# Kernel optimization log

Hardware: AMD Instinct MI355X
Metric: run time of the kernel (lower is better)

## Reference

```python
import jax, jax.numpy as jnp
import numpy as np

B, C, W = 8, 128, 4096
REDUCTION = 8
D = C // REDUCTION  # 16


def setup_inputs() -> dict:
    key = jax.random.key(0)
    ks = jax.random.split(key, 7)
    scale = 0.05
    return {
        "x": jax.random.normal(ks[0], (B, C, W), dtype=jnp.float32),
        "Wq": jax.random.normal(ks[1], (D, C), dtype=jnp.float32) * scale,
        "bq": jax.random.normal(ks[2], (D,), dtype=jnp.float32) * scale,
        "Wk": jax.random.normal(ks[3], (D, C), dtype=jnp.float32) * scale,
        "bk": jax.random.normal(ks[4], (D,), dtype=jnp.float32) * scale,
        "Wv": jax.random.normal(ks[5], (C, C), dtype=jnp.float32) * scale,
        "bv": jax.random.normal(ks[6], (C,), dtype=jnp.float32) * scale,
    }


def reference(x, Wq, bq, Wk, bk, Wv, bv):
    # 1x1 Conv1d == per-position linear over channel axis
    q = jnp.einsum('dc,bcw->bdw', Wq, x) + bq[None, :, None]   # [B, D, W]
    k = jnp.einsum('dc,bcw->bdw', Wk, x) + bk[None, :, None]   # [B, D, W]
    v = jnp.einsum('oc,bcw->bow', Wv, x) + bv[None, :, None]   # [B, C, W]
    scale = D ** (-0.5)
    # scores[b,i,j] = q[b,:,i] . k[b,:,j]
    scores = jnp.einsum('bdi,bdj->bij', q, k) * scale          # [B, W, W]
    attn = jax.nn.softmax(scores, axis=-1)
    # torch.bmm(value, attn): context[b,c,w] = sum_j v[b,c,j] * attn[b,j,w]
    context = jnp.einsum('bcj,bjw->bcw', v, attn)              # [B, C, W]
    return context + x
```

## Files before the change

kernel.cpp:

```cpp
#include <hip/hip_runtime.h>

#define B_ 8
#define C_ 128
#define W_ 4096
#define D_ 16
#define SCALE2 0.3606737602222409f

typedef short bf16x8 __attribute__((ext_vector_type(8)));
typedef float f32x4 __attribute__((ext_vector_type(4)));
typedef float f32x16 __attribute__((ext_vector_type(16)));

__device__ __forceinline__ unsigned short f2bf(float f) {
    unsigned int u = __float_as_uint(f);
    u += 0x7fffu + ((u >> 16) & 1u);
    return (unsigned short)(u >> 16);
}
__device__ __forceinline__ float bf2f(unsigned short h) {
    return __uint_as_float(((unsigned int)h) << 16);
}
__device__ __forceinline__ unsigned int pk2bf(float lo, float hi) {
    return __builtin_amdgcn_perm(__float_as_uint(hi), __float_as_uint(lo), 0x07060302u);
}
__device__ __forceinline__ bf16x8 uint4_as_bf8(uint4 u) {
    union { uint4 u; bf16x8 v; } t;
    t.u = u;
    return t.v;
}
__device__ __forceinline__ bf16x8 ld8w(const float* p, float sc) {
    float4 lo = *(const float4*)p, hi = *(const float4*)(p + 4);
    union { uint4 u; bf16x8 v; } t;
    t.u = make_uint4(pk2bf(lo.x * sc, lo.y * sc), pk2bf(lo.z * sc, lo.w * sc),
                     pk2bf(hi.x * sc, hi.y * sc), pk2bf(hi.z * sc, hi.w * sc));
    return t.v;
}
__device__ __forceinline__ uint4 exp2pkq(f32x16 s, int r0) {
    return make_uint4(
        pk2bf(__builtin_amdgcn_exp2f(s[r0+0]), __builtin_amdgcn_exp2f(s[r0+1])),
        pk2bf(__builtin_amdgcn_exp2f(s[r0+2]), __builtin_amdgcn_exp2f(s[r0+3])),
        pk2bf(__builtin_amdgcn_exp2f(s[r0+4]), __builtin_amdgcn_exp2f(s[r0+5])),
        pk2bf(__builtin_amdgcn_exp2f(s[r0+6]), __builtin_amdgcn_exp2f(s[r0+7])));
}
__device__ __forceinline__ int xswz(int j, int c8) {
    return c8 ^ (j & 7) ^ ((j >> 3) & 7);
}

__global__ __launch_bounds__(256) void proj(
    const float* __restrict__ x,
    const float* __restrict__ Wq, const float* __restrict__ Wk, const float* __restrict__ Wv,
    const float* __restrict__ bqp, const float* __restrict__ bkp, const float* __restrict__ bvp,
    unsigned short* __restrict__ qws2, unsigned short* __restrict__ kws2,
    unsigned short* __restrict__ vws2)
{
    __shared__ unsigned short xbf[32 * 128];
    __shared__ unsigned short outs[128 * 36];
    __shared__ unsigned short qk_s[2][32][24];

    int b  = blockIdx.x & 7;
    int j0 = (blockIdx.x >> 3) * 32;
    int jt = j0 >> 5;
    int tid = threadIdx.x;
    int wid = tid >> 6, lane = tid & 63, n = lane & 15, q4 = lane >> 4;

    {
        unsigned int* xbf32 = (unsigned int*)xbf;
#pragma unroll
        for (int i = 0; i < 8; i++) {
            int p = tid + 256 * i;
            int c2 = p >> 5;
            int j  = p & 31;
            const float* xp = x + (size_t)(b * C_ + 2 * c2) * W_ + j0 + j;
            float lo = xp[0];
            float hi = xp[W_];
            xbf32[j * 64 + xswz(j, c2 >> 2) * 4 + (c2 & 3)] = pk2bf(lo, hi);
        }
    }
    __syncthreads();

    const f32x4 zero = {0.f, 0.f, 0.f, 0.f};
    f32x4 accv[2][2]; f32x4 accqk = zero;
#pragma unroll
    for (int os = 0; os < 2; os++)
#pragma unroll
        for (int js = 0; js < 2; js++) accv[os][js] = zero;

    int isK = wid >> 1;
    int jsm = wid & 1;
    const float* wqk = isK ? Wk : Wq;
    const float qksc = isK ? 1.0f : SCALE2;

#pragma unroll
    for (int kk = 0; kk < 128; kk += 32) {
        bf16x8 av[2], aqkf, bx[2];
#pragma unroll
        for (int os = 0; os < 2; os++)
            av[os] = ld8w(Wv + (size_t)(wid * 32 + os * 16 + n) * 128 + kk + q4 * 8, 1.0f);
        aqkf = ld8w(wqk + (size_t)n * 128 + kk + q4 * 8, qksc);
#pragma unroll
        for (int js = 0; js < 2; js++) {
            int j = js * 16 + n;
            bx[js] = *(const bf16x8*)&xbf[j * 128 + xswz(j, (kk >> 3) + q4) * 8];
        }
#pragma unroll
        for (int os = 0; os < 2; os++)
#pragma unroll
            for (int js = 0; js < 2; js++)
                accv[os][js] = __builtin_amdgcn_mfma_f32_16x16x32_bf16(av[os], bx[js], accv[os][js], 0, 0, 0);
        accqk = __builtin_amdgcn_mfma_f32_16x16x32_bf16(aqkf, bx[jsm], accqk, 0, 0, 0);
    }

    {
        int pos = jsm * 16 + n;
        const float* bias = isK ? bkp : bqp;
        float bsc = isK ? 1.0f : SCALE2;
#pragma unroll
        for (int r = 0; r < 4; r++)
            qk_s[isK][pos][q4 * 4 + r] = f2bf(accqk[r] + bias[q4 * 4 + r] * bsc);
    }

    float bvv[2][4];
#pragma unroll
    for (int os = 0; os < 2; os++)
#pragma unroll
        for (int r = 0; r < 4; r++) bvv[os][r] = bvp[wid * 32 + os * 16 + q4 * 4 + r];
#pragma unroll
    for (int os = 0; os < 2; os++)
#pragma unroll
        for (int js = 0; js < 2; js++)
#pragma unroll
            for (int r = 0; r < 4; r++) {
                int c = wid * 32 + os * 16 + q4 * 4 + r;
                int j = js * 16 + n;
                outs[c * 36 + j] = f2bf(accv[os][js][r] + bvv[os][r]);
            }
    __syncthreads();

    if (tid < 128) {
        int qk = tid >> 6, hh = (tid >> 5) & 1, jl = tid & 31;
        uint4 v = *(const uint4*)&qk_s[qk][jl][hh * 8];
        unsigned short* dst = (qk ? kws2 : qws2)
            + (size_t)(b * 128 + jt) * 512 + hh * 256 + jl * 8;
        *(uint4*)dst = v;
    }
#pragma unroll
    for (int rep = 0; rep < 2; rep++) {
        int t = tid + rep * 256;
        int c = t & 127, sel = t >> 7;
        int jb = (sel >> 1) * 16 + (sel & 1) * 4;
        uint2 lo = *(const uint2*)&outs[c * 36 + jb];
        uint2 hi = *(const uint2*)&outs[c * 36 + jb + 8];
        *(uint4*)(vws2 + ((size_t)(b * 128 + jt) * 4 + sel) * 1024 + c * 8) =
            make_uint4(lo.x, lo.y, hi.x, hi.y);
    }
}

__global__ __launch_bounds__(256) void row_stats(
    const unsigned short* __restrict__ qws2, const unsigned short* __restrict__ kws2,
    float* __restrict__ rlp)
{
    int blk = blockIdx.x;
    int b = blk & 7;
    int j0 = ((blk >> 3) & 31) * 128;
    int wsp = blk >> 8;
    int tid = threadIdx.x;
    int wid = tid >> 6, lane = tid & 63, wl = lane & 31, h = lane >> 5;

    const unsigned short* qb = qws2 + (size_t)b * 65536;
    const unsigned short* kb = kws2 + (size_t)b * 65536;
    int jt = (j0 >> 5) + wid;

    bf16x8 aq = *(const bf16x8*)(qb + (size_t)jt * 512 + h * 256 + wl * 8);
    f32x16 zero16 = {0.f,0.f,0.f,0.f,0.f,0.f,0.f,0.f,0.f,0.f,0.f,0.f,0.f,0.f,0.f,0.f};

    float lt[16];
#pragma unroll
    for (int r = 0; r < 16; r++) lt[r] = 0.f;

    bf16x8 bkc = *(const bf16x8*)(kb + (size_t)(wsp * 32) * 512 + h * 256 + wl * 8);
    for (int t = 0; t < 32; t++) {
        f32x16 s = __builtin_amdgcn_mfma_f32_32x32x16_bf16(aq, bkc, zero16, 0, 0, 0);
        int tn = wsp * 32 + ((t + 1) & 31);
        bkc = *(const bf16x8*)(kb + (size_t)tn * 512 + h * 256 + wl * 8);
#pragma unroll
        for (int r = 0; r < 16; r++) lt[r] += __builtin_amdgcn_exp2f(s[r]);
    }
#pragma unroll
    for (int mask = 1; mask < 32; mask <<= 1)
#pragma unroll
        for (int r = 0; r < 16; r++) lt[r] += __shfl_xor(lt[r], mask, 64);
    if (wl == 0) {
#pragma unroll
        for (int g = 0; g < 4; g++) {
            f32x4 v = {lt[4*g+0], lt[4*g+1], lt[4*g+2], lt[4*g+3]};
            *(f32x4*)(rlp + (size_t)wsp * 32768 + (size_t)b * W_ + j0 + wid * 32 + 4 * h + 8 * g) = v;
        }
    }
}

__global__ __launch_bounds__(256) void vscale(unsigned short* __restrict__ vws2,
                                              const float* __restrict__ rlp)
{
    __shared__ float rl[16];
    int bi = blockIdx.x;
    int g0 = bi * 256;
    int kf = (g0 >> 8) & 1, jt = (g0 >> 9) & 127, b = g0 >> 16;
    int tid = threadIdx.x;
    if (tid < 16) {
        int idx = b * W_ + jt * 32 + kf * 16 + tid;
        float l = rlp[idx] + rlp[32768 + idx] + rlp[65536 + idx] + rlp[98304 + idx];
        rl[tid] = 1.0f / l;
    }
    __syncthreads();

    int g = g0 + tid;
    int hh = (g >> 7) & 1;
    float4 r0 = *(const float4*)&rl[4 * hh];
    float4 r1 = *(const float4*)&rl[4 * hh + 8];
    uint4 v = *(const uint4*)(vws2 + (size_t)g * 8);
    unsigned int o0 = pk2bf(bf2f((unsigned short)(v.x & 0xffffu)) * r0.x,
                            bf2f((unsigned short)(v.x >> 16))     * r0.y);
    unsigned int o1 = pk2bf(bf2f((unsigned short)(v.y & 0xffffu)) * r0.z,
                            bf2f((unsigned short)(v.y >> 16))     * r0.w);
    unsigned int o2 = pk2bf(bf2f((unsigned short)(v.z & 0xffffu)) * r1.x,
                            bf2f((unsigned short)(v.z >> 16))     * r1.y);
    unsigned int o3 = pk2bf(bf2f((unsigned short)(v.w & 0xffffu)) * r1.z,
                            bf2f((unsigned short)(v.w >> 16))     * r1.w);
    *(uint4*)(vws2 + (size_t)g * 8) = make_uint4(o0, o1, o2, o3);
}

__global__ __launch_bounds__(512, 4) void attn_out(
    const float* __restrict__ x, const unsigned short* __restrict__ qws2,
    const unsigned short* __restrict__ kws2, const unsigned short* __restrict__ vws2,
    float* __restrict__ out)
{
    __shared__ uint4 p_lds[2][1024];
    __shared__ float red[128 * 68];

    int b  = blockIdx.x & 7;
    int w0 = (blockIdx.x >> 3) * 64;
    int tid = threadIdx.x;
    int wid = tid >> 6, lane = tid & 63, wl = lane & 31, h = lane >> 5;
    int cq = wid >> 1, kh = wid & 1;

    const unsigned short* qb  = qws2 + (size_t)b * 65536;
    const unsigned short* kb  = kws2 + (size_t)b * 65536;
    const uint4* vtb4 = (const uint4*)(vws2 + (size_t)b * 524288) + h * 128 + (cq * 32 + wl);
    const int qoff = h * 256 + wl * 8;

    bf16x8 bk = *(const bf16x8*)(kb + (size_t)((w0 >> 5) + kh) * 512 + h * 256 + wl * 8);

    f32x16 zero16 = {0.f,0.f,0.f,0.f,0.f,0.f,0.f,0.f,0.f,0.f,0.f,0.f,0.f,0.f,0.f,0.f};
    f32x16 acc[2];
    acc[0] = zero16; acc[1] = zero16;

    const int wbase = cq * 256 + h * 64 + kh * 32 + wl;
    const int rbase = kh * 512 + h * 64 + wl;

    bf16x8 aq = *(const bf16x8*)(qb + (size_t)cq * 512 + qoff);
    uint4 vfA[4], vfB[4];
#pragma unroll
    for (int kf = 0; kf < 4; kf++)
        vfA[kf] = vtb4[(size_t)(kh * 4 + kf) * 256];
    {
        f32x16 s = __builtin_amdgcn_mfma_f32_32x32x16_bf16(aq, bk, zero16, 0, 0, 0);
        aq = *(const bf16x8*)(qb + (size_t)(4 + cq) * 512 + qoff);
        p_lds[0][wbase]       = exp2pkq(s, 0);
        p_lds[0][wbase + 128] = exp2pkq(s, 8);
    }
    __syncthreads();

#define STEP(IT, CUR, VC, VN)                                                        \
    {                                                                                \
        const int it_ = (IT);                                                        \
        int kgb = ((it_ + 1) & 31) * 8 + kh * 4;                                     \
        _Pragma("unroll") for (int kf = 0; kf < 4; kf++)                             \
            VN[kf] = vtb4[(size_t)(kgb + kf) * 256];                                 \
        f32x16 s = __builtin_amdgcn_mfma_f32_32x32x16_bf16(aq, bk, zero16, 0, 0, 0); \
        aq = *(const bf16x8*)(qb + (size_t)(((it_ + 2) & 31) * 4 + cq) * 512 + qoff);\
        __builtin_amdgcn_s_setprio(1);                                               \
        _Pragma("unroll") for (int kf = 0; kf < 4; kf++) {                           \
            bf16x8 af = uint4_as_bf8(VC[kf]);                                        \
            _Pragma("unroll") for (int nt = 0; nt < 2; nt++) {                       \
                bf16x8 bp = uint4_as_bf8(p_lds[CUR][rbase + kf * 128 + nt * 32]);    \
                acc[nt] = __builtin_amdgcn_mfma_f32_32x32x16_bf16(af, bp, acc[nt], 0, 0, 0); \
            }                                                                        \
        }                                                                            \
        __builtin_amdgcn_s_setprio(0);                                               \
        p_lds[(CUR) ^ 1][wbase]       = exp2pkq(s, 0);                               \
        p_lds[(CUR) ^ 1][wbase + 128] = exp2pkq(s, 8);                               \
        __syncthreads();                                                             \
    }

    for (int i2 = 0; i2 < 16; i2++) {
        STEP(2 * i2,     0, vfA, vfB);
        STEP(2 * i2 + 1, 1, vfB, vfA);
    }
#undef STEP

#define CROW(r) (cq * 32 + ((r) & 3) + 8 * ((r) >> 2) + 4 * h)
    if (kh == 1) {
#pragma unroll
        for (int nt = 0; nt < 2; nt++)
#pragma unroll
            for (int r = 0; r < 16; r++)
                red[CROW(r) * 68 + nt * 32 + wl] = acc[nt][r];
    }
    __syncthreads();
    if (kh == 0) {
#pragma unroll
        for (int nt = 0; nt < 2; nt++)
#pragma unroll
            for (int r = 0; r < 16; r++) {
                int o = CROW(r) * 68 + nt * 32 + wl;
                red[o] += acc[nt][r];
            }
    }
#undef CROW
    __syncthreads();

#pragma unroll
    for (int u = 0; u < 4; u++) {
        int k = tid + 512 * u;
        int c = k >> 4, wseg = (k & 15) * 4;
        size_t gidx = (size_t)(b * C_ + c) * W_ + w0 + wseg;
        float4 xv = *(const float4*)(x + gidx);
        const float* sp = &red[c * 68 + wseg];
        *(float4*)(out + gidx) = make_float4(sp[0] + xv.x, sp[1] + xv.y, sp[2] + xv.z, sp[3] + xv.w);
    }
}

extern "C" void kernel_launch(void* const* d_in, const int* in_sizes, int n_in,
                              void* d_out, int out_size, void* d_ws, size_t ws_size,
                              hipStream_t stream)
{
    const float* x  = (const float*)d_in[0];
    const float* Wq = (const float*)d_in[1];
    const float* bq = (const float*)d_in[2];
    const float* Wk = (const float*)d_in[3];
    const float* bk = (const float*)d_in[4];
    const float* Wv = (const float*)d_in[5];
    const float* bv = (const float*)d_in[6];
    float* out = (float*)d_out;

    unsigned short* qws2 = (unsigned short*)d_ws;
    unsigned short* kws2 = qws2 + (size_t)524288;
    unsigned short* vws2 = kws2 + (size_t)524288;
    float* rlp = (float*)(vws2 + (size_t)4194304);

    proj<<<1024, 256, 0, stream>>>(x, Wq, Wk, Wv, bq, bk, bv, qws2, kws2, vws2);
    row_stats<<<1024, 256, 0, stream>>>(qws2, kws2, rlp);
    vscale<<<2048, 256, 0, stream>>>(vws2, rlp);
    attn_out<<<512, 512, 0, stream>>>(x, qws2, kws2, vws2, out);
}
```

Before: 162.0 us.

## Process two key tiles per barrier in attention output loop

```diff
diff --git a/kernel.cpp b/kernel.cpp
--- a/kernel.cpp
+++ b/kernel.cpp
@@ -232,8 +232,9 @@
     const unsigned short* __restrict__ kws2, const unsigned short* __restrict__ vws2,
     float* __restrict__ out)
 {
-    __shared__ uint4 p_lds[2][1024];
-    __shared__ float red[128 * 68];
+    __shared__ __align__(16) unsigned char smem[65536];
+    uint4* p_u4 = (uint4*)smem;
+    float* red  = (float*)smem;
 
     int b  = blockIdx.x & 7;
     int w0 = (blockIdx.x >> 3) * 64;
@@ -255,46 +256,70 @@
     const int wbase = cq * 256 + h * 64 + kh * 32 + wl;
     const int rbase = kh * 512 + h * 64 + wl;
 
-    bf16x8 aq = *(const bf16x8*)(qb + (size_t)cq * 512 + qoff);
-    uint4 vfA[4], vfB[4];
-#pragma unroll
-    for (int kf = 0; kf < 4; kf++)
-        vfA[kf] = vtb4[(size_t)(kh * 4 + kf) * 256];
+#define QT(IT) ((const bf16x8*)(qb + (size_t)((((IT) & 31) * 4 + cq)) * 512 + qoff))
+#define VG(IT, KF) ((size_t)((((IT) & 31) * 8) + kh * 4 + (KF)) * 256)
+
+    bf16x8 aqA = *QT(0);
+    bf16x8 aqB = *QT(1);
+    uint4 vfX[4], vfY[4], vfZ[4];
+#pragma unroll
+    for (int kf = 0; kf < 4; kf++) vfX[kf] = vtb4[VG(0, kf)];
     {
-        f32x16 s = __builtin_amdgcn_mfma_f32_32x32x16_bf16(aq, bk, zero16, 0, 0, 0);
-        aq = *(const bf16x8*)(qb + (size_t)(4 + cq) * 512 + qoff);
-        p_lds[0][wbase]       = exp2pkq(s, 0);
-        p_lds[0][wbase + 128] = exp2pkq(s, 8);
-    }
-    __syncthreads();
-
-#define STEP(IT, CUR, VC, VN)                                                        \
+        f32x16 s0 = __builtin_amdgcn_mfma_f32_32x32x16_bf16(aqA, bk, zero16, 0, 0, 0);
+        f32x16 s1 = __builtin_amdgcn_mfma_f32_32x32x16_bf16(aqB, bk, zero16, 0, 0, 0);
+        aqA = *QT(2);
+        aqB = *QT(3);
+        p_u4[wbase]              = exp2pkq(s0, 0);
+        p_u4[wbase + 128]        = exp2pkq(s0, 8);
+        p_u4[1024 + wbase]       = exp2pkq(s1, 0);
+        p_u4[1024 + wbase + 128] = exp2pkq(s1, 8);
+    }
+    __syncthreads();
+
+#define SUPER(T, RD, WR)                                                             \
     {                                                                                \
-        const int it_ = (IT);                                                        \
-        int kgb = ((it_ + 1) & 31) * 8 + kh * 4;                                     \
-        _Pragma("unroll") for (int kf = 0; kf < 4; kf++)                             \
-            VN[kf] = vtb4[(size_t)(kgb + kf) * 256];                                 \
-        f32x16 s = __builtin_amdgcn_mfma_f32_32x32x16_bf16(aq, bk, zero16, 0, 0, 0); \
-        aq = *(const bf16x8*)(qb + (size_t)(((it_ + 2) & 31) * 4 + cq) * 512 + qoff);\
+        const int t_ = (T);                                                          \
+        _Pragma("unroll") for (int kf = 0; kf < 4; kf++) {                           \
+            vfY[kf] = vtb4[VG(2 * t_ + 1, kf)];                                      \
+            vfZ[kf] = vtb4[VG(2 * t_ + 2, kf)];                                      \
+        }                                                                            \
+        f32x16 s0 = __builtin_amdgcn_mfma_f32_32x32x16_bf16(aqA, bk, zero16, 0, 0, 0); \
+        f32x16 s1 = __builtin_amdgcn_mfma_f32_32x32x16_bf16(aqB, bk, zero16, 0, 0, 0); \
+        aqA = *QT(2 * t_ + 4);                                                       \
+        aqB = *QT(2 * t_ + 5);                                                       \
         __builtin_amdgcn_s_setprio(1);                                               \
         _Pragma("unroll") for (int kf = 0; kf < 4; kf++) {                           \
-            bf16x8 af = uint4_as_bf8(VC[kf]);                                        \
+            bf16x8 af = uint4_as_bf8(vfX[kf]);                                       \
             _Pragma("unroll") for (int nt = 0; nt < 2; nt++) {                       \
-                bf16x8 bp = uint4_as_bf8(p_lds[CUR][rbase + kf * 128 + nt * 32]);    \
+                bf16x8 bp = uint4_as_bf8(p_u4[(RD) + rbase + kf * 128 + nt * 32]);   \
                 acc[nt] = __builtin_amdgcn_mfma_f32_32x32x16_bf16(af, bp, acc[nt], 0, 0, 0); \
             }                                                                        \
         }                                                                            \
         __builtin_amdgcn_s_setprio(0);                                               \
-        p_lds[(CUR) ^ 1][wbase]       = exp2pkq(s, 0);                               \
-        p_lds[(CUR) ^ 1][wbase + 128] = exp2pkq(s, 8);                               \
+        p_u4[(WR) + wbase]       = exp2pkq(s0, 0);                                   \
+        p_u4[(WR) + wbase + 128] = exp2pkq(s0, 8);                                   \
+        __builtin_amdgcn_s_setprio(1);                                               \
+        _Pragma("unroll") for (int kf = 0; kf < 4; kf++) {                           \
+            bf16x8 af = uint4_as_bf8(vfY[kf]);                                       \
+            _Pragma("unroll") for (int nt = 0; nt < 2; nt++) {                       \
+                bf16x8 bp = uint4_as_bf8(p_u4[(RD) + 1024 + rbase + kf * 128 + nt * 32]); \
+                acc[nt] = __builtin_amdgcn_mfma_f32_32x32x16_bf16(af, bp, acc[nt], 0, 0, 0); \
+            }                                                                        \
+        }                                                                            \
+        __builtin_amdgcn_s_setprio(0);                                               \
+        p_u4[(WR) + 1024 + wbase]       = exp2pkq(s1, 0);                            \
+        p_u4[(WR) + 1024 + wbase + 128] = exp2pkq(s1, 8);                            \
+        _Pragma("unroll") for (int kf = 0; kf < 4; kf++) vfX[kf] = vfZ[kf];          \
         __syncthreads();                                                             \
     }
 
-    for (int i2 = 0; i2 < 16; i2++) {
-        STEP(2 * i2,     0, vfA, vfB);
-        STEP(2 * i2 + 1, 1, vfB, vfA);
-    }
-#undef STEP
+    for (int t2 = 0; t2 < 8; t2++) {
+        SUPER(2 * t2,     0,    2048);
+        SUPER(2 * t2 + 1, 2048, 0);
+    }
+#undef SUPER
+#undef QT
+#undef VG
 
 #define CROW(r) (cq * 32 + ((r) & 3) + 8 * ((r) >> 2) + 4 * h)
     if (kh == 1) {
```

After: 163.2 us. About the same (+0.7%).
